# Kernel optimization log

Measured on AMD Instinct MI355X. Metric: run time of the kernel, lower is better.

The kernel has to match this reference:

```python
import jax, jax.numpy as jnp
import numpy as np
import math

EMBED_DIM = 128
NUM_HEADS = 16
HEAD_DIM = EMBED_DIM // NUM_HEADS  # = 8 = n_wires of the quantum circuit


def setup_inputs() -> dict:
    key = jax.random.key(0)
    k1, k2, k3 = jax.random.split(key, 3)
    B, S = 4, 2048
    x = jax.random.normal(k1, (B, S, EMBED_DIM), dtype=jnp.float32)
    # shared trainable RX angles of the single q_layer (applied to every head)
    theta = jax.random.normal(k2, (HEAD_DIM,), dtype=jnp.float32)
    w_out = jax.random.normal(k3, (EMBED_DIM, EMBED_DIM), dtype=jnp.float32) / math.sqrt(EMBED_DIM)
    mask = jnp.ones((B, S), dtype=jnp.int32)
    return {"x": x, "theta": theta, "w_out": w_out, "mask": mask}


def quantum_linear(x_head, theta):
    # Circuit: RX(x_i) encode + RX(theta_i) on wire i, CNOT chain (i, i+1),
    # then <Z_j>. For product state |psi_i> = RX(phi_i)|0>, <Z_i> = cos(phi_i),
    # and the CNOT chain gives final <Z_j> = prod_{i<=j} cos(phi_i).
    phi = x_head + theta  # [..., D] broadcast over leading dims
    return jnp.cumprod(jnp.cos(phi), axis=-1)


def reference(x, theta, w_out, mask):
    B, S, E = x.shape
    H, D = NUM_HEADS, HEAD_DIM
    xs = x.reshape(B, S, H, D)
    q = quantum_linear(xs, theta).transpose(0, 2, 1, 3)  # [B, H, S, D]; k = v = q
    scores = jnp.einsum("bhsd,bhtd->bhst", q, q) / math.sqrt(D)
    scores = jnp.where(mask[:, None, None, :] == 0, -1e9, scores)
    probs = jax.nn.softmax(scores, axis=-1)  # dropout is identity in eval
    attn = jnp.einsum("bhst,bhtd->bhsd", probs, q)
    attn = attn.transpose(0, 2, 1, 3).reshape(B, S, E)
    return attn @ w_out.T
```

## Files before the change

kernel.cpp:

```cpp
#include <hip/hip_runtime.h>
#include <hip/hip_bf16.h>
#include <hip/hip_fp16.h>

#define NB 4
#define NS 2048
#define NE 128
#define NH 16
#define ND 8

typedef __attribute__((ext_vector_type(8))) _Float16 half8;
typedef __attribute__((ext_vector_type(4))) float f32x4;

#define VSTRIDE 2056

__device__ __forceinline__ unsigned int pkrtz(float a, float b) {
    typedef __fp16 fp16v2 __attribute__((ext_vector_type(2)));
    union { fp16v2 h; unsigned int u; } v;
    v.h = __builtin_amdgcn_cvt_pkrtz(a, b);
    return v.u;
}
__device__ __forceinline__ unsigned short f2h(float a) {
    return __half_as_ushort(__float2half(a));
}
__device__ __forceinline__ half8 mk_half8(unsigned u0, unsigned u1,
                                          unsigned u2, unsigned u3) {
    union { half8 h; unsigned u[4]; } v;
    v.u[0] = u0; v.u[1] = u1; v.u[2] = u2; v.u[3] = u3;
    return v.h;
}

__global__ __launch_bounds__(512) void attn_kernel(
        const float* __restrict__ x,
        const float* __restrict__ theta,
        const int* __restrict__ mask,
        unsigned short* __restrict__ mid) {
    __shared__ unsigned short qhl[NS * ND + 24];
    __shared__ unsigned short vT[9 * VSTRIDE];
    __shared__ float kb[NS];

    const int bid = blockIdx.x;
    const int bh = bid >> 3;
    const int b = bh >> 4, h = bh & (NH - 1);
    const int meighth = bid & 7;
    const int tid = threadIdx.x;

    const float SC = 0.71421629f;

    float th[ND];
#pragma unroll
    for (int d = 0; d < ND; d++) th[d] = theta[d];

    for (int idx = tid; idx < 1024; idx += 512) {
        int chs = idx >> 4, i = idx & 15;
        int ta = 4 * (i >> 2) + 2 * (i & 1) + 16 * ((i >> 1) & 1);
        int r0 = chs * 32 + ta, r1 = r0 + 1;
        float p0[ND], p1[ND];
        {
            const float* xp = x + ((size_t)(b * NS + r0) * NE + h * ND);
            float4 a = *(const float4*)xp, c = *(const float4*)(xp + 4);
            float p = 1.f;
            p *= cosf(a.x + th[0]); p0[0] = p; p *= cosf(a.y + th[1]); p0[1] = p;
            p *= cosf(a.z + th[2]); p0[2] = p; p *= cosf(a.w + th[3]); p0[3] = p;
            p *= cosf(c.x + th[4]); p0[4] = p; p *= cosf(c.y + th[5]); p0[5] = p;
            p *= cosf(c.z + th[6]); p0[6] = p; p *= cosf(c.w + th[7]); p0[7] = p;
        }
        {
            const float* xp = x + ((size_t)(b * NS + r1) * NE + h * ND);
            float4 a = *(const float4*)xp, c = *(const float4*)(xp + 4);
            float p = 1.f;
            p *= cosf(a.x + th[0]); p1[0] = p; p *= cosf(a.y + th[1]); p1[1] = p;
            p *= cosf(a.z + th[2]); p1[2] = p; p *= cosf(a.w + th[3]); p1[3] = p;
            p *= cosf(c.x + th[4]); p1[4] = p; p *= cosf(c.y + th[5]); p1[5] = p;
            p *= cosf(c.z + th[6]); p1[6] = p; p *= cosf(c.w + th[7]); p1[7] = p;
        }
        uint4 qa, qb;
        qa.x = pkrtz(p0[0] * SC, p0[1] * SC);
        qa.y = pkrtz(p0[2] * SC, p0[3] * SC);
        qa.z = pkrtz(p0[4] * SC, p0[5] * SC);
        qa.w = pkrtz(p0[6] * SC, p0[7] * SC);
        qb.x = pkrtz(p1[0] * SC, p1[1] * SC);
        qb.y = pkrtz(p1[2] * SC, p1[3] * SC);
        qb.z = pkrtz(p1[4] * SC, p1[5] * SC);
        qb.w = pkrtz(p1[6] * SC, p1[7] * SC);
        *(uint4*)&qhl[r0 * ND] = qa;
        *(uint4*)&qhl[r1 * ND] = qb;
#pragma unroll
        for (int d = 0; d < ND; d++)
            *(unsigned int*)&vT[d * VSTRIDE + chs * 32 + 2 * i] = pkrtz(p0[d], p1[d]);
        *(unsigned int*)&vT[8 * VSTRIDE + chs * 32 + 2 * i] = 0x3C003C00u;
    }
    for (int i = tid; i < NS; i += 512)
        kb[i] = mask[b * NS + i] ? 0.f : -30000.f;
    if (tid < 24) qhl[NS * ND + tid] = 0;
    __syncthreads();

    const int wave = tid >> 6, lane = tid & 63;
    const int quad = lane >> 4, l15 = lane & 15;
    const int mbase = meighth * 256 + wave * 32;

    half8 hz = {0, 0, 0, 0, 0, 0, 0, 0};
    half8 bm0 = quad ? hz : *(const half8*)&qhl[(mbase + l15) * ND];
    half8 bm1 = quad ? hz : *(const half8*)&qhl[(mbase + 16 + l15) * ND];

    const int vrow = (l15 < 9) ? l15 : 8;
    const unsigned short* vbase = &vT[vrow * VSTRIDE];

    f32x4 O0 = {0.f, 0.f, 0.f, 0.f}, O1 = {0.f, 0.f, 0.f, 0.f};
    for (int ch = 0; ch < 64; ch++) {
        int tb = ch * 32;
        half8 at0 = *(const half8*)&qhl[(tb + l15) * ND + quad * 8];
        half8 at1 = *(const half8*)&qhl[(tb + 16 + l15) * ND + quad * 8];
        half8 vf  = *(const half8*)&vbase[tb + quad * 8];
        f32x4 C0 = *(const f32x4*)&kb[tb + quad * 4];
        f32x4 C1 = *(const f32x4*)&kb[tb + 16 + quad * 4];

        f32x4 s00 = __builtin_amdgcn_mfma_f32_16x16x32_f16(at0, bm0, C0, 0, 0, 0);
        f32x4 s01 = __builtin_amdgcn_mfma_f32_16x16x32_f16(at0, bm1, C0, 0, 0, 0);
        f32x4 s10 = __builtin_amdgcn_mfma_f32_16x16x32_f16(at1, bm0, C1, 0, 0, 0);
        f32x4 s11 = __builtin_amdgcn_mfma_f32_16x16x32_f16(at1, bm1, C1, 0, 0, 0);

        half8 pA0 = mk_half8(
            pkrtz(__builtin_amdgcn_exp2f(s00[0]), __builtin_amdgcn_exp2f(s00[1])),
            pkrtz(__builtin_amdgcn_exp2f(s00[2]), __builtin_amdgcn_exp2f(s00[3])),
            pkrtz(__builtin_amdgcn_exp2f(s10[0]), __builtin_amdgcn_exp2f(s10[1])),
            pkrtz(__builtin_amdgcn_exp2f(s10[2]), __builtin_amdgcn_exp2f(s10[3])));
        half8 pA1 = mk_half8(
            pkrtz(__builtin_amdgcn_exp2f(s01[0]), __builtin_amdgcn_exp2f(s01[1])),
            pkrtz(__builtin_amdgcn_exp2f(s01[2]), __builtin_amdgcn_exp2f(s01[3])),
            pkrtz(__builtin_amdgcn_exp2f(s11[0]), __builtin_amdgcn_exp2f(s11[1])),
            pkrtz(__builtin_amdgcn_exp2f(s11[2]), __builtin_amdgcn_exp2f(s11[3])));

        O0 = __builtin_amdgcn_mfma_f32_16x16x32_f16(pA0, vf, O0, 0, 0, 0);
        O1 = __builtin_amdgcn_mfma_f32_16x16x32_f16(pA1, vf, O1, 0, 0, 0);
    }

#pragma unroll
    for (int mt = 0; mt < 2; mt++) {
        f32x4 O = mt ? O1 : O0;
#pragma unroll
        for (int r = 0; r < 4; r++) {
            float lsum = __shfl(O[r], (lane & 48) | 8, 64);
            float v = O[r] / lsum;
            if (l15 < ND) {
                int m = mbase + mt * 16 + quad * 4 + r;
                mid[(size_t)(b * NS + m) * NE + h * ND + l15] = f2h(v);
            }
        }
    }
}

__global__ __launch_bounds__(256) void proj_kernel(
        const unsigned short* __restrict__ mid,
        const float* __restrict__ w,
        float* __restrict__ out) {
    __shared__ unsigned short wf[NE * 136];
    __shared__ unsigned short am[32 * 136];
    const int rb = blockIdx.x * 32;
    const int tid = threadIdx.x;

    for (int i = tid; i < 2048; i += 256) {
        const float* wp = w + i * 8;
        float4 a = *(const float4*)wp, c = *(const float4*)(wp + 4);
        uint4 pk;
        pk.x = pkrtz(a.x, a.y); pk.y = pkrtz(a.z, a.w);
        pk.z = pkrtz(c.x, c.y); pk.w = pkrtz(c.z, c.w);
        int n = i >> 4, k8 = (i & 15) * 8;
        *(uint4*)&wf[n * 136 + k8] = pk;
    }
    for (int i = tid; i < 512; i += 256) {
        int r = i >> 4, k8 = (i & 15) * 8;
        uint4 v = *(const uint4*)&mid[(size_t)(rb + r) * NE + k8];
        *(uint4*)&am[r * 136 + k8] = v;
    }
    __syncthreads();

    const int wave = tid >> 6, lane = tid & 63;
    const int quad = lane >> 4, l15 = lane & 15;
    const int mt = wave & 1, nh = wave >> 1;

    half8 af[4];
#pragma unroll
    for (int kt = 0; kt < 4; kt++)
        af[kt] = *(const half8*)&am[(mt * 16 + l15) * 136 + kt * 32 + quad * 8];

#pragma unroll
    for (int nt = 0; nt < 4; nt++) {
        int n0 = (nh * 4 + nt) * 16;
        f32x4 acc = {0.f, 0.f, 0.f, 0.f};
#pragma unroll
        for (int kt = 0; kt < 4; kt++) {
            half8 bf = *(const half8*)&wf[(n0 + l15) * 136 + kt * 32 + quad * 8];
            acc = __builtin_amdgcn_mfma_f32_16x16x32_f16(af[kt], bf, acc, 0, 0, 0);
        }
#pragma unroll
        for (int r = 0; r < 4; r++)
            out[(size_t)(rb + mt * 16 + quad * 4 + r) * NE + n0 + l15] = acc[r];
    }
}

extern "C" void kernel_launch(void* const* d_in, const int* in_sizes, int n_in,
                              void* d_out, int out_size, void* d_ws, size_t ws_size,
                              hipStream_t stream) {
    const float* x     = (const float*)d_in[0];
    const float* theta = (const float*)d_in[1];
    const float* w_out = (const float*)d_in[2];
    const int*   mask  = (const int*)d_in[3];
    float* out = (float*)d_out;

    unsigned short* mid16 = (unsigned short*)d_ws;

    attn_kernel<<<NB * NH * 8, 512, 0, stream>>>(x, theta, mask, mid16);
    proj_kernel<<<NB * NS / 32, 256, 0, stream>>>(mid16, w_out, out);
}
```

Baseline: 102.1 us.

## Split attention key range into two phases to halve LDS footprint

Keys and values are now staged in two halves of 1024 rows, each loaded, synced and consumed in turn, which halves the shared-memory footprint. The mask bias buffer is gone: masking now zeroes V rows and the row-sum column instead of adding a large negative bias. Query fragments are computed directly from global x in registers rather than read back from LDS. The goal is more resident blocks per CU through a smaller LDS allocation and a launch-bounds occupancy hint, at the cost of an extra barrier per phase and less overlap between loading and compute.

```diff
diff --git a/kernel.cpp b/kernel.cpp
--- a/kernel.cpp
+++ b/kernel.cpp
@@ -8,10 +8,12 @@
 #define NH 16
 #define ND 8
 
+#define THALF 1024
+#define NCH 32
+#define VSTRIDE 1032
+
 typedef __attribute__((ext_vector_type(8))) _Float16 half8;
 typedef __attribute__((ext_vector_type(4))) float f32x4;
-
-#define VSTRIDE 2056
 
 __device__ __forceinline__ unsigned int pkrtz(float a, float b) {
     typedef __fp16 fp16v2 __attribute__((ext_vector_type(2)));
@@ -28,15 +30,31 @@
     v.u[0] = u0; v.u[1] = u1; v.u[2] = u2; v.u[3] = u3;
     return v.h;
 }
-
-__global__ __launch_bounds__(512) void attn_kernel(
+__device__ __forceinline__ half8 u4_half8(uint4 u) {
+    union { uint4 u4; half8 h; } v; v.u4 = u; return v.h;
+}
+
+__device__ __forceinline__ void qrow(const float* __restrict__ xp,
+                                     const float* th, float* p) {
+    float4 a = *(const float4*)xp, c = *(const float4*)(xp + 4);
+    float t = 1.f;
+    t *= cosf(a.x + th[0]); p[0] = t;
+    t *= cosf(a.y + th[1]); p[1] = t;
+    t *= cosf(a.z + th[2]); p[2] = t;
+    t *= cosf(a.w + th[3]); p[3] = t;
+    t *= cosf(c.x + th[4]); p[4] = t;
+    t *= cosf(c.y + th[5]); p[5] = t;
+    t *= cosf(c.z + th[6]); p[6] = t;
+    t *= cosf(c.w + th[7]); p[7] = t;
+}
+
+__global__ __launch_bounds__(512, 8) void attn_kernel(
         const float* __restrict__ x,
         const float* __restrict__ theta,
         const int* __restrict__ mask,
         unsigned short* __restrict__ mid) {
-    __shared__ unsigned short qhl[NS * ND + 24];
+    __shared__ unsigned short qhl[THALF * ND + 24];
     __shared__ unsigned short vT[9 * VSTRIDE];
-    __shared__ float kb[NS];
 
     const int bid = blockIdx.x;
     const int bh = bid >> 3;
@@ -50,88 +68,93 @@
 #pragma unroll
     for (int d = 0; d < ND; d++) th[d] = theta[d];
 
-    for (int idx = tid; idx < 1024; idx += 512) {
-        int chs = idx >> 4, i = idx & 15;
-        int ta = 4 * (i >> 2) + 2 * (i & 1) + 16 * ((i >> 1) & 1);
-        int r0 = chs * 32 + ta, r1 = r0 + 1;
-        float p0[ND], p1[ND];
-        {
-            const float* xp = x + ((size_t)(b * NS + r0) * NE + h * ND);
-            float4 a = *(const float4*)xp, c = *(const float4*)(xp + 4);
-            float p = 1.f;
-            p *= cosf(a.x + th[0]); p0[0] = p; p *= cosf(a.y + th[1]); p0[1] = p;
-            p *= cosf(a.z + th[2]); p0[2] = p; p *= cosf(a.w + th[3]); p0[3] = p;
-            p *= cosf(c.x + th[4]); p0[4] = p; p *= cosf(c.y + th[5]); p0[5] = p;
-            p *= cosf(c.z + th[6]); p0[6] = p; p *= cosf(c.w + th[7]); p0[7] = p;
-        }
-        {
-            const float* xp = x + ((size_t)(b * NS + r1) * NE + h * ND);
-            float4 a = *(const float4*)xp, c = *(const float4*)(xp + 4);
-            float p = 1.f;
-            p *= cosf(a.x + th[0]); p1[0] = p; p *= cosf(a.y + th[1]); p1[1] = p;
-            p *= cosf(a.z + th[2]); p1[2] = p; p *= cosf(a.w + th[3]); p1[3] = p;
-            p *= cosf(c.x + th[4]); p1[4] = p; p *= cosf(c.y + th[5]); p1[5] = p;
-            p *= cosf(c.z + th[6]); p1[6] = p; p *= cosf(c.w + th[7]); p1[7] = p;
-        }
-        uint4 qa, qb;
-        qa.x = pkrtz(p0[0] * SC, p0[1] * SC);
-        qa.y = pkrtz(p0[2] * SC, p0[3] * SC);
-        qa.z = pkrtz(p0[4] * SC, p0[5] * SC);
-        qa.w = pkrtz(p0[6] * SC, p0[7] * SC);
-        qb.x = pkrtz(p1[0] * SC, p1[1] * SC);
-        qb.y = pkrtz(p1[2] * SC, p1[3] * SC);
-        qb.z = pkrtz(p1[4] * SC, p1[5] * SC);
-        qb.w = pkrtz(p1[6] * SC, p1[7] * SC);
-        *(uint4*)&qhl[r0 * ND] = qa;
-        *(uint4*)&qhl[r1 * ND] = qb;
-#pragma unroll
-        for (int d = 0; d < ND; d++)
-            *(unsigned int*)&vT[d * VSTRIDE + chs * 32 + 2 * i] = pkrtz(p0[d], p1[d]);
-        *(unsigned int*)&vT[8 * VSTRIDE + chs * 32 + 2 * i] = 0x3C003C00u;
-    }
-    for (int i = tid; i < NS; i += 512)
-        kb[i] = mask[b * NS + i] ? 0.f : -30000.f;
-    if (tid < 24) qhl[NS * ND + tid] = 0;
-    __syncthreads();
-
     const int wave = tid >> 6, lane = tid & 63;
     const int quad = lane >> 4, l15 = lane & 15;
     const int mbase = meighth * 256 + wave * 32;
 
+    if (tid < 24) qhl[THALF * ND + tid] = 0;
+
     half8 hz = {0, 0, 0, 0, 0, 0, 0, 0};
-    half8 bm0 = quad ? hz : *(const half8*)&qhl[(mbase + l15) * ND];
-    half8 bm1 = quad ? hz : *(const half8*)&qhl[(mbase + 16 + l15) * ND];
+    half8 bm0, bm1;
+    {
+        float pm[ND];
+        uint4 qa, qb;
+        qrow(x + ((size_t)(b * NS + mbase + l15) * NE + h * ND), th, pm);
+        qa.x = pkrtz(pm[0] * SC, pm[1] * SC);
+        qa.y = pkrtz(pm[2] * SC, pm[3] * SC);
+        qa.z = pkrtz(pm[4] * SC, pm[5] * SC);
+        qa.w = pkrtz(pm[6] * SC, pm[7] * SC);
+        qrow(x + ((size_t)(b * NS + mbase + 16 + l15) * NE + h * ND), th, pm);
+        qb.x = pkrtz(pm[0] * SC, pm[1] * SC);
+        qb.y = pkrtz(pm[2] * SC, pm[3] * SC);
+        qb.z = pkrtz(pm[4] * SC, pm[5] * SC);
+        qb.w = pkrtz(pm[6] * SC, pm[7] * SC);
+        bm0 = quad ? hz : u4_half8(qa);
+        bm1 = quad ? hz : u4_half8(qb);
+    }
 
     const int vrow = (l15 < 9) ? l15 : 8;
     const unsigned short* vbase = &vT[vrow * VSTRIDE];
 
     f32x4 O0 = {0.f, 0.f, 0.f, 0.f}, O1 = {0.f, 0.f, 0.f, 0.f};
-    for (int ch = 0; ch < 64; ch++) {
-        int tb = ch * 32;
-        half8 at0 = *(const half8*)&qhl[(tb + l15) * ND + quad * 8];
-        half8 at1 = *(const half8*)&qhl[(tb + 16 + l15) * ND + quad * 8];
-        half8 vf  = *(const half8*)&vbase[tb + quad * 8];
-        f32x4 C0 = *(const f32x4*)&kb[tb + quad * 4];
-        f32x4 C1 = *(const f32x4*)&kb[tb + 16 + quad * 4];
-
-        f32x4 s00 = __builtin_amdgcn_mfma_f32_16x16x32_f16(at0, bm0, C0, 0, 0, 0);
-        f32x4 s01 = __builtin_amdgcn_mfma_f32_16x16x32_f16(at0, bm1, C0, 0, 0, 0);
-        f32x4 s10 = __builtin_amdgcn_mfma_f32_16x16x32_f16(at1, bm0, C1, 0, 0, 0);
-        f32x4 s11 = __builtin_amdgcn_mfma_f32_16x16x32_f16(at1, bm1, C1, 0, 0, 0);
-
-        half8 pA0 = mk_half8(
-            pkrtz(__builtin_amdgcn_exp2f(s00[0]), __builtin_amdgcn_exp2f(s00[1])),
-            pkrtz(__builtin_amdgcn_exp2f(s00[2]), __builtin_amdgcn_exp2f(s00[3])),
-            pkrtz(__builtin_amdgcn_exp2f(s10[0]), __builtin_amdgcn_exp2f(s10[1])),
-            pkrtz(__builtin_amdgcn_exp2f(s10[2]), __builtin_amdgcn_exp2f(s10[3])));
-        half8 pA1 = mk_half8(
-            pkrtz(__builtin_amdgcn_exp2f(s01[0]), __builtin_amdgcn_exp2f(s01[1])),
-            pkrtz(__builtin_amdgcn_exp2f(s01[2]), __builtin_amdgcn_exp2f(s01[3])),
-            pkrtz(__builtin_amdgcn_exp2f(s11[0]), __builtin_amdgcn_exp2f(s11[1])),
-            pkrtz(__builtin_amdgcn_exp2f(s11[2]), __builtin_amdgcn_exp2f(s11[3])));
-
-        O0 = __builtin_amdgcn_mfma_f32_16x16x32_f16(pA0, vf, O0, 0, 0, 0);
-        O1 = __builtin_amdgcn_mfma_f32_16x16x32_f16(pA1, vf, O1, 0, 0, 0);
+    const f32x4 zc = {0.f, 0.f, 0.f, 0.f};
+
+    for (int ph = 0; ph < 2; ph++) {
+        {
+            int chs = tid >> 4, i = tid & 15;
+            int ta = 4 * (i >> 2) + 2 * (i & 1) + 16 * ((i >> 1) & 1);
+            int r0 = chs * 32 + ta, r1 = r0 + 1;
+            int g0 = ph * THALF + r0;
+            float p0[ND], p1[ND];
+            qrow(x + ((size_t)(b * NS + g0) * NE + h * ND), th, p0);
+            qrow(x + ((size_t)(b * NS + g0 + 1) * NE + h * ND), th, p1);
+            float mz0 = mask[b * NS + g0] ? 1.f : 0.f;
+            float mz1 = mask[b * NS + g0 + 1] ? 1.f : 0.f;
+            uint4 qa, qb;
+            qa.x = pkrtz(p0[0] * SC, p0[1] * SC);
+            qa.y = pkrtz(p0[2] * SC, p0[3] * SC);
+            qa.z = pkrtz(p0[4] * SC, p0[5] * SC);
+            qa.w = pkrtz(p0[6] * SC, p0[7] * SC);
+            qb.x = pkrtz(p1[0] * SC, p1[1] * SC);
+            qb.y = pkrtz(p1[2] * SC, p1[3] * SC);
+            qb.z = pkrtz(p1[4] * SC, p1[5] * SC);
+            qb.w = pkrtz(p1[6] * SC, p1[7] * SC);
+            *(uint4*)&qhl[r0 * ND] = qa;
+            *(uint4*)&qhl[r1 * ND] = qb;
+#pragma unroll
+            for (int d = 0; d < ND; d++)
+                *(unsigned int*)&vT[d * VSTRIDE + chs * 32 + 2 * i] =
+                    pkrtz(p0[d] * mz0, p1[d] * mz1);
+            *(unsigned int*)&vT[8 * VSTRIDE + chs * 32 + 2 * i] = pkrtz(mz0, mz1);
+        }
+        __syncthreads();
+
+        for (int ch = 0; ch < NCH; ch++) {
+            int tb = ch * 32;
+            half8 at0 = *(const half8*)&qhl[(tb + l15) * ND + quad * 8];
+            half8 at1 = *(const half8*)&qhl[(tb + 16 + l15) * ND + quad * 8];
+            half8 vf  = *(const half8*)&vbase[tb + quad * 8];
+
+            f32x4 s00 = __builtin_amdgcn_mfma_f32_16x16x32_f16(at0, bm0, zc, 0, 0, 0);
+            f32x4 s01 = __builtin_amdgcn_mfma_f32_16x16x32_f16(at0, bm1, zc, 0, 0, 0);
+            f32x4 s10 = __builtin_amdgcn_mfma_f32_16x16x32_f16(at1, bm0, zc, 0, 0, 0);
+            f32x4 s11 = __builtin_amdgcn_mfma_f32_16x16x32_f16(at1, bm1, zc, 0, 0, 0);
+
+            half8 pA0 = mk_half8(
+                pkrtz(__builtin_amdgcn_exp2f(s00[0]), __builtin_amdgcn_exp2f(s00[1])),
+                pkrtz(__builtin_amdgcn_exp2f(s00[2]), __builtin_amdgcn_exp2f(s00[3])),
+                pkrtz(__builtin_amdgcn_exp2f(s10[0]), __builtin_amdgcn_exp2f(s10[1])),
+                pkrtz(__builtin_amdgcn_exp2f(s10[2]), __builtin_amdgcn_exp2f(s10[3])));
+            half8 pA1 = mk_half8(
+                pkrtz(__builtin_amdgcn_exp2f(s01[0]), __builtin_amdgcn_exp2f(s01[1])),
+                pkrtz(__builtin_amdgcn_exp2f(s01[2]), __builtin_amdgcn_exp2f(s01[3])),
+                pkrtz(__builtin_amdgcn_exp2f(s11[0]), __builtin_amdgcn_exp2f(s11[1])),
+                pkrtz(__builtin_amdgcn_exp2f(s11[2]), __builtin_amdgcn_exp2f(s11[3])));
+
+            O0 = __builtin_amdgcn_mfma_f32_16x16x32_f16(pA0, vf, O0, 0, 0, 0);
+            O1 = __builtin_amdgcn_mfma_f32_16x16x32_f16(pA1, vf, O1, 0, 0, 0);
+        }
+        __syncthreads();
     }
 
 #pragma unroll
```

After: 116.6 us. +14.2%, slower.
